# Kernel tuning notes

Hardware: AMD Instinct MI355X
Metric: run time of the kernel (lower is better)

Reference implementation:

```python
import jax, jax.numpy as jnp
import numpy as np

B, S, H, NH, HD = 2, 2048, 2048, 16, 128
E, TOPK, I = 8, 2, 2048
EPS = 1e-5
ROPE_THETA = 10000.0


def setup_inputs() -> dict:
    key = jax.random.key(0)
    ks = jax.random.split(key, 11)
    s = 0.02
    return {
        "hidden_states": jax.random.normal(ks[0], (B, S, H), jnp.float32),
        "position_ids": jnp.broadcast_to(jnp.arange(S, dtype=jnp.int32), (B, S)),
        "rms1_w": jnp.ones((H,), jnp.float32),
        "rms2_w": jnp.ones((H,), jnp.float32),
        "q_w": jax.random.normal(ks[1], (H, H), jnp.float32) * s,
        "k_w": jax.random.normal(ks[2], (H, H), jnp.float32) * s,
        "v_w": jax.random.normal(ks[3], (H, H), jnp.float32) * s,
        "o_w": jax.random.normal(ks[4], (H, H), jnp.float32) * s,
        "router_w": jax.random.normal(ks[5], (H, E), jnp.float32) * s,
        "w1": jax.random.normal(ks[6], (E, H, I), jnp.float32) * s,
        "w2": jax.random.normal(ks[7], (E, I, H), jnp.float32) * s,
        "w3": jax.random.normal(ks[8], (E, H, I), jnp.float32) * s,
    }


def rmsnorm(x, w):
    var = jnp.mean(x * x, axis=-1, keepdims=True)
    return (x * jax.lax.rsqrt(var + EPS)) * w


def rope(x, pos):
    # x: [B,S,NH,HD], pos: [B,S]
    half = HD // 2
    inv_freq = 1.0 / (ROPE_THETA ** (jnp.arange(0, half, dtype=jnp.float32) / half))
    ang = pos.astype(jnp.float32)[..., None] * inv_freq  # [B,S,half]
    cos = jnp.cos(ang)[:, :, None, :]
    sin = jnp.sin(ang)[:, :, None, :]
    x1, x2 = x[..., :half], x[..., half:]
    return jnp.concatenate([x1 * cos - x2 * sin, x2 * cos + x1 * sin], axis=-1)


def attention(x, pos, q_w, k_w, v_w, o_w):
    q = (x @ q_w).reshape(B, S, NH, HD)
    k = (x @ k_w).reshape(B, S, NH, HD)
    v = (x @ v_w).reshape(B, S, NH, HD)
    q = rope(q, pos)
    k = rope(k, pos)
    scores = jnp.einsum("bqhd,bkhd->bhqk", q, k) / np.sqrt(HD).astype(np.float32)
    causal = jnp.tril(jnp.ones((S, S), bool))
    scores = jnp.where(causal, scores, jnp.finfo(scores.dtype).min)
    probs = jax.nn.softmax(scores, axis=-1)
    ctx = jnp.einsum("bhqk,bkhd->bqhd", probs, v).reshape(B, S, H)
    return ctx @ o_w


def moe(x, router_w, w1, w2, w3):
    t = x.reshape(B * S, H)
    probs = jax.nn.softmax(t @ router_w, axis=-1)  # [T,E]
    top_v, top_i = jax.lax.top_k(probs, TOPK)
    top_v = top_v / jnp.sum(top_v, axis=-1, keepdims=True)
    T = B * S
    coeff = jnp.zeros((T, E), x.dtype).at[jnp.arange(T)[:, None], top_i].set(top_v)
    y = jnp.zeros((T, H), x.dtype)
    for e in range(E):  # fixed small expert loop
        h = jax.nn.silu(t @ w1[e]) * (t @ w3[e])
        y = y + coeff[:, e:e + 1] * (h @ w2[e])
    return y.reshape(B, S, H)


def reference(hidden_states, position_ids, rms1_w, rms2_w, q_w, k_w, v_w, o_w,
              router_w, w1, w2, w3):
    residual = hidden_states
    h = rmsnorm(hidden_states, rms1_w).astype(hidden_states.dtype)
    h = attention(h, position_ids, q_w, k_w, v_w, o_w)
    h = residual + h
    residual = h
    h = rmsnorm(h, rms2_w).astype(h.dtype)
    h = moe(h, router_w, w1, w2, w3)
    return residual + h
```

## Files before the change

### kernel.cpp

```cpp
#include <hip/hip_runtime.h>
#include <hip/hip_bf16.h>

constexpr int CB   = 2;
constexpr int CS   = 2048;
constexpr int CH   = 2048;
constexpr int CNH  = 16;
constexpr int CHD  = 128;
constexpr int CE   = 8;
constexpr int CI   = 2048;
constexpr int CT   = CB * CS;
constexpr int CQKV = 3 * CH;

typedef __attribute__((ext_vector_type(8))) short short8;
typedef __attribute__((ext_vector_type(4))) float float4v;
typedef __attribute__((ext_vector_type(4))) unsigned short ushort4v;
typedef unsigned int uint32;

__device__ __forceinline__ float bf2f(unsigned short u) {
    union { unsigned int i; float f; } x; x.i = ((unsigned int)u) << 16; return x.f;
}
__device__ __forceinline__ unsigned short f2bf(float f) {
    union { float f; unsigned int i; } x; x.f = f;
    unsigned int r = x.i + 0x7fffu + ((x.i >> 16) & 1u);
    return (unsigned short)(r >> 16);
}
__device__ __forceinline__ uint32 packpair(uint32 r0, uint32 r1) {
    return __builtin_amdgcn_perm(r1, r0, 0x07060302u);
}
__device__ __forceinline__ uint32 rnebits(float f) {
    uint32 u = __float_as_uint(f);
    return u + 0x7fffu + ((u >> 16) & 1u);
}
__device__ __forceinline__ void split2(float f0, float f1, uint32& h, uint32& l) {
    uint32 r0 = rnebits(f0), r1 = rnebits(f1);
    h = packpair(r0, r1);
    float d0 = f0 - __uint_as_float(r0 & 0xffff0000u);
    float d1 = f1 - __uint_as_float(r1 & 0xffff0000u);
    l = packpair(rnebits(d0), rnebits(d1));
}
__device__ __forceinline__ void rne16_store(const float* fv, unsigned short* dst) {
    uint32 h[8];
    #pragma unroll
    for (int p = 0; p < 8; p++) h[p] = packpair(rnebits(fv[2 * p]), rnebits(fv[2 * p + 1]));
    ((uint4*)dst)[0] = make_uint4(h[0], h[1], h[2], h[3]);
    ((uint4*)dst)[1] = make_uint4(h[4], h[5], h[6], h[7]);
}

template<int MODE>
__global__ __launch_bounds__(256) void rmsnorm_k(const float* __restrict__ x,
                                                 const float* __restrict__ w,
                                                 unsigned short* __restrict__ o1,
                                                 unsigned short* __restrict__ o2) {
    const int row = blockIdx.x;
    const float* xr = x + (size_t)row * CH;
    const int base = threadIdx.x * 8;
    float4 v0 = *(const float4*)(xr + base);
    float4 v1 = *(const float4*)(xr + base + 4);
    float ss = v0.x*v0.x + v0.y*v0.y + v0.z*v0.z + v0.w*v0.w
             + v1.x*v1.x + v1.y*v1.y + v1.z*v1.z + v1.w*v1.w;
    #pragma unroll
    for (int o = 1; o < 64; o <<= 1) ss += __shfl_xor(ss, o);
    __shared__ float ps[4];
    if ((threadIdx.x & 63) == 0) ps[threadIdx.x >> 6] = ss;
    __syncthreads();
    const float scale = rsqrtf((ps[0] + ps[1] + ps[2] + ps[3]) / (float)CH + 1e-5f);
    float4 w0 = *(const float4*)(w + base);
    float4 w1 = *(const float4*)(w + base + 4);
    float r[8] = {v0.x * scale * w0.x, v0.y * scale * w0.y, v0.z * scale * w0.z, v0.w * scale * w0.w,
                  v1.x * scale * w1.x, v1.y * scale * w1.y, v1.z * scale * w1.z, v1.w * scale * w1.w};
    if (MODE == 1) {
        rne16_store(r, o1 + (size_t)row * CH + base);
    } else {
        uint32 h[4], l[4];
        #pragma unroll
        for (int p = 0; p < 4; p++) split2(r[2 * p], r[2 * p + 1], h[p], l[p]);
        *(uint4*)(o1 + (size_t)row * CH + base) = make_uint4(h[0], h[1], h[2], h[3]);
        *(uint4*)(o2 + (size_t)row * CH + base) = make_uint4(l[0], l[1], l[2], l[3]);
    }
}

__global__ void rope_tab_k(float2* __restrict__ tab) {
    int i = blockIdx.x * 256 + threadIdx.x;
    int p = i >> 6, j = i & 63;
    double inv = pow(10000.0, -(double)j / 64.0);
    float invf = (float)inv;
    float angf = (float)p * invf;
    double da = (double)angf;
    tab[i] = make_float2((float)cos(da), (float)sin(da));
}

__global__ __launch_bounds__(256) void rope_k(unsigned short* __restrict__ qh,
                                              unsigned short* __restrict__ ql,
                                              const int* __restrict__ pos,
                                              const float2* __restrict__ tab) {
    int i = blockIdx.x * 256 + threadIdx.x;
    if (i >= CT * CNH * 64) return;
    int t = i >> 10, hj = i & 1023, hh = hj >> 6, j = hj & 63;
    float2 cs = tab[(size_t)pos[t] * 64 + j];
    unsigned short* qhp = qh + (size_t)t * CQKV + hh * CHD;
    unsigned short* qlp = ql + (size_t)t * CQKV + hh * CHD;
    #pragma unroll
    for (int s = 0; s < 2; s++) {
        unsigned short* hp = qhp + s * CH;
        unsigned short* lp = qlp + s * CH;
        float x1 = bf2f(hp[j]) + bf2f(lp[j]);
        float x2 = bf2f(hp[j + 64]) + bf2f(lp[j + 64]);
        float y1 = x1 * cs.x - x2 * cs.y;
        float y2 = x2 * cs.x + x1 * cs.y;
        uint32 r1 = rnebits(y1), r2 = rnebits(y2);
        hp[j]      = (unsigned short)(r1 >> 16);
        hp[j + 64] = (unsigned short)(r2 >> 16);
        lp[j]      = f2bf(y1 - __uint_as_float(r1 & 0xffff0000u));
        lp[j + 64] = f2bf(y2 - __uint_as_float(r2 & 0xffff0000u));
    }
}

template<int NMAT>
__global__ __launch_bounds__(256) void conv_k(const float* __restrict__ S0,
                                              const float* __restrict__ S1,
                                              unsigned short* __restrict__ D) {
    __shared__ float t[64][65];
    const int n0 = blockIdx.x * 64, k0 = blockIdx.y * 64, e = blockIdx.z;
    const size_t esrc = (size_t)e * 2048 * 2048;
    const int cc = threadIdx.x & 63, r4 = threadIdx.x >> 6;
    const int nl = threadIdx.x >> 2, q = threadIdx.x & 3;
    #pragma unroll
    for (int s = 0; s < NMAT; s++) {
        const float* S = s ? S1 : S0;
        __syncthreads();
        #pragma unroll
        for (int j = 0; j < 16; j++) {
            const int row = j * 4 + r4;
            t[cc][row] = S[esrc + (size_t)(k0 + row) * 2048 + n0 + cc];
        }
        __syncthreads();
        const int orow = (NMAT == 2) ? (2 * (n0 + nl) + s) : (n0 + nl);
        unsigned short* dp = D + (size_t)e * (NMAT * 2048) * 2048 + (size_t)orow * 2048 + k0 + q * 16;
        float fv[16];
        #pragma unroll
        for (int j = 0; j < 16; j++) fv[j] = t[nl][q * 16 + j];
        rne16_store(fv, dp);
    }
}

template<int NMAT>
__global__ __launch_bounds__(256) void convs_k(const float* __restrict__ S0,
                                               const float* __restrict__ S1,
                                               const float* __restrict__ S2,
                                               unsigned short* __restrict__ Dh,
                                               unsigned short* __restrict__ Dl) {
    __shared__ float t[64][65];
    const int n0 = blockIdx.x * 64, k0 = blockIdx.y * 64, z = blockIdx.z;
    const float* S = S0;
    if (NMAT == 3) S = (z == 0) ? S0 : ((z == 1) ? S1 : S2);
    const int cc = threadIdx.x & 63, r4 = threadIdx.x >> 6;
    #pragma unroll
    for (int j = 0; j < 16; j++) {
        const int row = j * 4 + r4;
        t[cc][row] = S[(size_t)(k0 + row) * 2048 + n0 + cc];
    }
    __syncthreads();
    const int nl = threadIdx.x >> 2, q = threadIdx.x & 3;
    float fv[16];
    #pragma unroll
    for (int j = 0; j < 16; j++) fv[j] = t[nl][q * 16 + j];
    uint32 h[8], l[8];
    #pragma unroll
    for (int p = 0; p < 8; p++) split2(fv[2 * p], fv[2 * p + 1], h[p], l[p]);
    const size_t off = (size_t)(z * 2048 + n0 + nl) * 2048 + k0 + q * 16;
    ((uint4*)(Dh + off))[0] = make_uint4(h[0], h[1], h[2], h[3]);
    ((uint4*)(Dh + off))[1] = make_uint4(h[4], h[5], h[6], h[7]);
    ((uint4*)(Dl + off))[0] = make_uint4(l[0], l[1], l[2], l[3]);
    ((uint4*)(Dl + off))[1] = make_uint4(l[4], l[5], l[6], l[7]);
}

template<int MODE>
__global__ __launch_bounds__(256) void sgemm_k(
    const unsigned short* __restrict__ Ahg, const unsigned short* __restrict__ Alg, int lda,
    const unsigned short* __restrict__ Bhg, const unsigned short* __restrict__ Blg, int K,
    unsigned short* __restrict__ Ch, unsigned short* __restrict__ Cl,
    float* __restrict__ Cf, int ldc,
    const float* __restrict__ resid, float* __restrict__ C2) {
    __shared__ unsigned short AhS[128][40], AlS[128][40], BhS[128][40], BlS[128][40];
    const int mt = blockIdx.x, nt = blockIdx.y, tid = threadIdx.x;
    const int m0 = mt * 128;
    const int srow = tid >> 1, shalf = tid & 1;
    const unsigned short* ah = Ahg + (size_t)(m0 + srow) * lda + shalf * 16;
    const unsigned short* al = Alg + (size_t)(m0 + srow) * lda + shalf * 16;
    const unsigned short* bhp = Bhg + (size_t)(nt * 128 + srow) * K + shalf * 16;
    const unsigned short* blp = Blg + (size_t)(nt * 128 + srow) * K + shalf * 16;
    const int lane = tid & 63, lr = lane & 15, lg = lane >> 4;
    const int wr = (tid >> 7) & 1, wc = (tid >> 6) & 1;

    float4v acc[4][4];
    #pragma unroll
    for (int m = 0; m < 4; m++)
        #pragma unroll
        for (int n = 0; n < 4; n++) acc[m][n] = (float4v){0.f, 0.f, 0.f, 0.f};

    short8 rah0 = *(const short8*)(ah),     rah1 = *(const short8*)(ah + 8);
    short8 ral0 = *(const short8*)(al),     ral1 = *(const short8*)(al + 8);
    short8 rbh0 = *(const short8*)(bhp),    rbh1 = *(const short8*)(bhp + 8);
    short8 rbl0 = *(const short8*)(blp),    rbl1 = *(const short8*)(blp + 8);

    for (int k0 = 0; k0 < K; k0 += 32) {
        __syncthreads();
        *(short8*)(&AhS[srow][shalf * 16])     = rah0;
        *(short8*)(&AhS[srow][shalf * 16 + 8]) = rah1;
        *(short8*)(&AlS[srow][shalf * 16])     = ral0;
        *(short8*)(&AlS[srow][shalf * 16 + 8]) = ral1;
        *(short8*)(&BhS[srow][shalf * 16])     = rbh0;
        *(short8*)(&BhS[srow][shalf * 16 + 8]) = rbh1;
        *(short8*)(&BlS[srow][shalf * 16])     = rbl0;
        *(short8*)(&BlS[srow][shalf * 16 + 8]) = rbl1;
        if (k0 + 32 < K) {
            rah0 = *(const short8*)(ah + k0 + 32);  rah1 = *(const short8*)(ah + k0 + 40);
            ral0 = *(const short8*)(al + k0 + 32);  ral1 = *(const short8*)(al + k0 + 40);
            rbh0 = *(const short8*)(bhp + k0 + 32); rbh1 = *(const short8*)(bhp + k0 + 40);
            rbl0 = *(const short8*)(blp + k0 + 32); rbl1 = *(const short8*)(blp + k0 + 40);
        }
        __syncthreads();
        short8 fah[4], fal[4], fbh[4], fbl[4];
        #pragma unroll
        for (int m = 0; m < 4; m++) {
            fah[m] = *(const short8*)(&AhS[wr * 64 + m * 16 + lr][lg * 8]);
            fal[m] = *(const short8*)(&AlS[wr * 64 + m * 16 + lr][lg * 8]);
        }
        #pragma unroll
        for (int n = 0; n < 4; n++) {
            fbh[n] = *(const short8*)(&BhS[wc * 64 + n * 16 + lr][lg * 8]);
            fbl[n] = *(const short8*)(&BlS[wc * 64 + n * 16 + lr][lg * 8]);
        }
        #pragma unroll
        for (int n = 0; n < 4; n++)
            #pragma unroll
            for (int m = 0; m < 4; m++) {
                acc[m][n] = __builtin_amdgcn_mfma_f32_16x16x32_bf16(fal[m], fbh[n], acc[m][n], 0, 0, 0);
                acc[m][n] = __builtin_amdgcn_mfma_f32_16x16x32_bf16(fah[m], fbl[n], acc[m][n], 0, 0, 0);
                acc[m][n] = __builtin_amdgcn_mfma_f32_16x16x32_bf16(fah[m], fbh[n], acc[m][n], 0, 0, 0);
            }
    }
    #pragma unroll
    for (int m = 0; m < 4; m++) {
        const int rb = wr * 64 + m * 16 + lg * 4;
        #pragma unroll
        for (int n = 0; n < 4; n++) {
            const int ccol = nt * 128 + wc * 64 + n * 16 + lr;
            #pragma unroll
            for (int r = 0; r < 4; r++) {
                const size_t idx = (size_t)(m0 + rb + r) * ldc + ccol;
                if (MODE == 1) {
                    const float v = acc[m][n][r] + resid[idx];
                    Cf[idx] = v;
                    C2[idx] = v;
                } else {
                    const float v = acc[m][n][r];
                    uint32 rr = rnebits(v);
                    Ch[idx] = (unsigned short)(rr >> 16);
                    Cl[idx] = f2bf(v - __uint_as_float(rr & 0xffff0000u));
                }
            }
        }
    }
}

template<int MODE>
__global__ __launch_bounds__(256) void gemm_k(
    const unsigned short* __restrict__ A, int lda,
    const unsigned short* __restrict__ Bt, int K, int Ne,
    void* __restrict__ Cp, int ldc,
    const int* __restrict__ cnt, const int* __restrict__ tokl,
    const float* __restrict__ gatel, const int* __restrict__ pb) {
    __shared__ unsigned short As[128][40];
    __shared__ unsigned short Bs[128][40];
    const int nt = blockIdx.x, mt = blockIdx.y, e = blockIdx.z;
    const int m0 = mt * 128;
    const int c = cnt[e];
    if (m0 >= c) return;
    const int valid = (c - m0 < 128) ? (c - m0) : 128;
    const int tid = threadIdx.x;
    const int srow = tid >> 1, shalf = tid & 1;
    size_t gr;
    if (MODE == 2) {
        const int idx = m0 + (srow < valid ? srow : valid - 1);
        gr = (size_t)tokl[e * 4096 + idx];
    } else {
        const int rr = m0 + srow;
        gr = (size_t)(pb[e] + (rr < c ? rr : c - 1));
    }
    const unsigned short* a_src = A + gr * (size_t)lda + shalf * 16;
    const unsigned short* b_src = Bt + (size_t)e * Ne * K + (size_t)(nt * 128 + srow) * K + shalf * 16;
    const int lane = tid & 63, lr = lane & 15, lg = lane >> 4;
    const int wr = (tid >> 7) & 1, wc = (tid >> 6) & 1;

    float4v acc[4][4];
    #pragma unroll
    for (int m = 0; m < 4; m++)
        #pragma unroll
        for (int n = 0; n < 4; n++) acc[m][n] = (float4v){0.f, 0.f, 0.f, 0.f};

    short8 ra0 = *(const short8*)(a_src);
    short8 ra1 = *(const short8*)(a_src + 8);
    short8 rb0 = *(const short8*)(b_src);
    short8 rb1 = *(const short8*)(b_src + 8);

    for (int k0 = 0; k0 < K; k0 += 32) {
        __syncthreads();
        *(short8*)(&As[srow][shalf * 16])     = ra0;
        *(short8*)(&As[srow][shalf * 16 + 8]) = ra1;
        *(short8*)(&Bs[srow][shalf * 16])     = rb0;
        *(short8*)(&Bs[srow][shalf * 16 + 8]) = rb1;
        if (k0 + 32 < K) {
            ra0 = *(const short8*)(a_src + k0 + 32);
            ra1 = *(const short8*)(a_src + k0 + 40);
            rb0 = *(const short8*)(b_src + k0 + 32);
            rb1 = *(const short8*)(b_src + k0 + 40);
        }
        __syncthreads();
        short8 af[4], bf[4];
        #pragma unroll
        for (int m = 0; m < 4; m++) af[m] = *(const short8*)(&As[wr * 64 + m * 16 + lr][lg * 8]);
        #pragma unroll
        for (int n = 0; n < 4; n++) bf[n] = *(const short8*)(&Bs[wc * 64 + n * 16 + lr][lg * 8]);
        #pragma unroll
        for (int n = 0; n < 4; n++)
            #pragma unroll
            for (int m = 0; m < 4; m++)
                acc[m][n] = __builtin_amdgcn_mfma_f32_16x16x32_bf16(af[m], bf[n], acc[m][n], 0, 0, 0);
    }

    #pragma unroll
    for (int m = 0; m < 4; m++) {
        const int rb = wr * 64 + m * 16 + lg * 4;
        #pragma unroll
        for (int n = 0; n < 4; n++) {
            const int col = nt * 128 + wc * 64 + n * 16 + lr;
            #pragma unroll
            for (int r = 0; r < 4; r++) {
                const int row = rb + r;
                const float v = acc[m][n][r];
                if (MODE == 2) {
                    const float other = __shfl_xor(v, 1);
                    if (!(lr & 1) && row < valid) {
                        const float g1 = v, g3 = other;
                        const float hsw = (g1 / (1.f + __expf(-g1))) * g3;
                        ((unsigned short*)Cp)[(size_t)(pb[e] + m0 + row) * ldc + (col >> 1)] = f2bf(hsw);
                    }
                } else {
                    if (row < valid) {
                        const int t = tokl[e * 4096 + m0 + row];
                        const float g = gatel[e * 4096 + m0 + row];
                        atomicAdd(((float*)Cp) + (size_t)t * ldc + col, v * g);
                    }
                }
            }
        }
    }
}

__global__ __launch_bounds__(256) void attn_k(const unsigned short* __restrict__ qh,
                                              const unsigned short* __restrict__ ql,
                                              unsigned short* __restrict__ ch,
                                              unsigned short* __restrict__ cl) {
    __shared__ unsigned short Ksh[32][136], Ksl[32][136];
    __shared__ unsigned short Vth[128][40], Vtl[128][40];
    const int bid = blockIdx.x;
    const int xcd = bid & 7, jj = bid >> 3;
    const int bh  = xcd * 4 + (jj >> 5);
    const int qb  = 31 - (jj & 31);
    const int h   = bh & 15, b = bh >> 4;
    const int tid = threadIdx.x;
    const int wave = tid >> 6, lane = tid & 63, lr = lane & 15, lg = lane >> 4;
    const size_t tb = (size_t)b * CS;
    const int q0 = qb * 64 + wave * 16;

    short8 qfh[4], qfl[4];
    {
        const size_t off = (tb + q0 + lr) * CQKV + h * CHD;
        #pragma unroll
        for (int c = 0; c < 4; c++) {
            qfh[c] = *(const short8*)(qh + off + c * 32 + lg * 8);
            qfl[c] = *(const short8*)(ql + off + c * 32 + lg * 8);
        }
    }
    float4v o[8];
    #pragma unroll
    for (int d = 0; d < 8; d++) o[d] = (float4v){0.f, 0.f, 0.f, 0.f};
    float m = -1e30f, l = 0.f;
    const float scl = 0.08838834764831845f;
    const int ntiles = 2 * (qb + 1);
    const int kk = tid >> 3, slot = tid & 7;
    const int vd = tid & 127, vhalf = tid >> 7;

    short8 pkh0, pkh1, pkl0, pkl1;
    unsigned short pth[16], ptl[16];
    {
        const size_t koff = (tb + kk) * CQKV + CH + h * CHD + slot * 16;
        pkh0 = *(const short8*)(qh + koff);
        pkh1 = *(const short8*)(qh + koff + 8);
        pkl0 = *(const short8*)(ql + koff);
        pkl1 = *(const short8*)(ql + koff + 8);
        const size_t voff = (tb + vhalf * 16) * CQKV + 2 * CH + h * CHD + vd;
        #pragma unroll
        for (int j = 0; j < 16; j++) {
            pth[j] = qh[voff + (size_t)j * CQKV];
            ptl[j] = ql[voff + (size_t)j * CQKV];
        }
    }

    for (int kt = 0; kt < ntiles; ++kt) {
        const int kv0 = kt * 32;
        __syncthreads();
        *(short8*)(&Ksh[kk][slot * 16])     = pkh0;
        *(short8*)(&Ksh[kk][slot * 16 + 8]) = pkh1;
        *(short8*)(&Ksl[kk][slot * 16])     = pkl0;
        *(short8*)(&Ksl[kk][slot * 16 + 8]) = pkl1;
        #pragma unroll
        for (int p = 0; p < 2; p++) {
            *(ushort4v*)(&Vth[vd][vhalf * 16 + p * 8])     = *(ushort4v*)(&pth[p * 8]);
            *(ushort4v*)(&Vth[vd][vhalf * 16 + p * 8 + 4]) = *(ushort4v*)(&pth[p * 8 + 4]);
            *(ushort4v*)(&Vtl[vd][vhalf * 16 + p * 8])     = *(ushort4v*)(&ptl[p * 8]);
            *(ushort4v*)(&Vtl[vd][vhalf * 16 + p * 8 + 4]) = *(ushort4v*)(&ptl[p * 8 + 4]);
        }
        if (kt + 1 < ntiles) {
            const int nv0 = kv0 + 32;
            const size_t koff = (tb + nv0 + kk) * CQKV + CH + h * CHD + slot * 16;
            pkh0 = *(const short8*)(qh + koff);
            pkh1 = *(const short8*)(qh + koff + 8);
            pkl0 = *(const short8*)(ql + koff);
            pkl1 = *(const short8*)(ql + koff + 8);
            const size_t voff = (tb + nv0 + vhalf * 16) * CQKV + 2 * CH + h * CHD + vd;
            #pragma unroll
            for (int j = 0; j < 16; j++) {
                pth[j] = qh[voff + (size_t)j * CQKV];
                ptl[j] = ql[voff + (size_t)j * CQKV];
            }
        }
        __syncthreads();

        float4v st0 = (float4v){0.f,0.f,0.f,0.f}, st1 = st0;
        #pragma unroll
        for (int c = 0; c < 4; c++) {
            short8 kah = *(const short8*)(&Ksh[lr][c * 32 + lg * 8]);
            short8 kal = *(const short8*)(&Ksl[lr][c * 32 + lg * 8]);
            short8 kbh = *(const short8*)(&Ksh[16 + lr][c * 32 + lg * 8]);
            short8 kbl = *(const short8*)(&Ksl[16 + lr][c * 32 + lg * 8]);
            st0 = __builtin_amdgcn_mfma_f32_16x16x32_bf16(kal, qfh[c], st0, 0, 0, 0);
            st0 = __builtin_amdgcn_mfma_f32_16x16x32_bf16(kah, qfl[c], st0, 0, 0, 0);
            st0 = __builtin_amdgcn_mfma_f32_16x16x32_bf16(kah, qfh[c], st0, 0, 0, 0);
            st1 = __builtin_amdgcn_mfma_f32_16x16x32_bf16(kbl, qfh[c], st1, 0, 0, 0);
            st1 = __builtin_amdgcn_mfma_f32_16x16x32_bf16(kbh, qfl[c], st1, 0, 0, 0);
            st1 = __builtin_amdgcn_mfma_f32_16x16x32_bf16(kbh, qfh[c], st1, 0, 0, 0);
        }
        float pv[8]; float pmax = -1e30f;
        const int qg = q0 + lr;
        #pragma unroll
        for (int f = 0; f < 2; f++) {
            #pragma unroll
            for (int r = 0; r < 4; r++) {
                const int kg = kv0 + f * 16 + lg * 4 + r;
                const float s = (kg <= qg) ? ((f ? st1[r] : st0[r]) * scl) : -1e30f;
                pv[f * 4 + r] = s;
                pmax = fmaxf(pmax, s);
            }
        }
        pmax = fmaxf(pmax, __shfl_xor(pmax, 16));
        pmax = fmaxf(pmax, __shfl_xor(pmax, 32));
        const float mnew = fmaxf(m, pmax);
        const float alpha = __expf(m - mnew);
        float sum = 0.f;
        #pragma unroll
        for (int i = 0; i < 8; i++) { const float p = __expf(pv[i] - mnew); pv[i] = p; sum += p; }
        sum += __shfl_xor(sum, 16);
        sum += __shfl_xor(sum, 32);
        l = l * alpha + sum;
        m = mnew;
        #pragma unroll
        for (int d = 0; d < 8; d++) o[d] *= alpha;
        short8 pfh, pfl;
        unsigned short* pfhp = (unsigned short*)&pfh;
        unsigned short* pflp = (unsigned short*)&pfl;
        #pragma unroll
        for (int j = 0; j < 8; j++) {
            const int srcl = (((lg & 1) * 2 + (j >> 2)) << 4) | lr;
            const float a0 = __shfl(pv[j & 3], srcl);
            const float a1 = __shfl(pv[4 + (j & 3)], srcl);
            const float sel = (lg >= 2) ? a1 : a0;
            uint32 r = rnebits(sel);
            pfhp[j] = (unsigned short)(r >> 16);
            float d = sel - __uint_as_float(r & 0xffff0000u);
            pflp[j] = (unsigned short)(rnebits(d) >> 16);
        }
        #pragma unroll
        for (int dt = 0; dt < 8; dt++) {
            short8 vh = *(const short8*)(&Vth[dt * 16 + lr][lg * 8]);
            short8 vl = *(const short8*)(&Vtl[dt * 16 + lr][lg * 8]);
            o[dt] = __builtin_amdgcn_mfma_f32_16x16x32_bf16(vl, pfh, o[dt], 0, 0, 0);
            o[dt] = __builtin_amdgcn_mfma_f32_16x16x32_bf16(vh, pfl, o[dt], 0, 0, 0);
            o[dt] = __builtin_amdgcn_mfma_f32_16x16x32_bf16(vh, pfh, o[dt], 0, 0, 0);
        }
    }
    const float inv = 1.f / l;
    const size_t coff = (tb + q0 + lr) * CH + h * CHD + lg * 4;
    #pragma unroll
    for (int dt = 0; dt < 8; dt++) {
        ushort4v wh, wl;
        #pragma unroll
        for (int r = 0; r < 4; r++) {
            const float v = o[dt][r] * inv;
            uint32 rr = rnebits(v);
            wh[r] = (unsigned short)(rr >> 16);
            wl[r] = f2bf(v - __uint_as_float(rr & 0xffff0000u));
        }
        *(ushort4v*)(ch + coff + dt * 16) = wh;
        *(ushort4v*)(cl + coff + dt * 16) = wl;
    }
}

__global__ __launch_bounds__(64) void router_k(const float* __restrict__ x,
                                               const float* __restrict__ wn,
                                               const float* __restrict__ rw,
                                               int* __restrict__ cnt, int* __restrict__ tok,
                                               float* __restrict__ gate) {
    const int t = blockIdx.x;
    const int lane = threadIdx.x;
    const float* xr = x + (size_t)t * CH;
    double ss = 0.0;
    double acc[8] = {0,0,0,0,0,0,0,0};
    for (int i = lane * 4; i < CH; i += 256) {
        float4 v = *(const float4*)(xr + i);
        float4 wv = *(const float4*)(wn + i);
        ss += (double)v.x*v.x + (double)v.y*v.y + (double)v.z*v.z + (double)v.w*v.w;
        float xs[4] = {v.x, v.y, v.z, v.w};
        float ws4[4] = {wv.x, wv.y, wv.z, wv.w};
        #pragma unroll
        for (int dd = 0; dd < 4; dd++) {
            const double xn = (double)xs[dd] * (double)ws4[dd];
            const float* rr = rw + (size_t)(i + dd) * CE;
            #pragma unroll
            for (int e2 = 0; e2 < 8; e2++) acc[e2] += xn * (double)rr[e2];
        }
    }
    #pragma unroll
    for (int o = 1; o < 64; o <<= 1) ss += __shfl_xor(ss, o);
    #pragma unroll
    for (int e2 = 0; e2 < 8; e2++) {
        #pragma unroll
        for (int o = 1; o < 64; o <<= 1) acc[e2] += __shfl_xor(acc[e2], o);
    }
    if (lane == 0) {
        const double scale = rsqrt(ss / (double)CH + 1e-5);
        int e0 = 0;
        #pragma unroll
        for (int e2 = 1; e2 < 8; e2++) if (acc[e2] > acc[e0]) e0 = e2;
        int e1 = (e0 == 0) ? 1 : 0;
        #pragma unroll
        for (int e2 = 0; e2 < 8; e2++) if (e2 != e0 && acc[e2] > acc[e1]) e1 = e2;
        const double dl = scale * (acc[e1] - acc[e0]);
        const double p1r = exp(dl);
        const float g0 = (float)(1.0 / (1.0 + p1r));
        const float g1 = (float)(p1r / (1.0 + p1r));
        int pos0 = atomicAdd(&cnt[e0], 1);
        tok[e0 * 4096 + pos0] = t; gate[e0 * 4096 + pos0] = g0;
        int pos1 = atomicAdd(&cnt[e1], 1);
        tok[e1 * 4096 + pos1] = t; gate[e1 * 4096 + pos1] = g1;
    }
}

__global__ void prefix_k(const int* __restrict__ cnt, int* __restrict__ pb) {
    if (threadIdx.x == 0 && blockIdx.x == 0) {
        int s = 0;
        for (int e = 0; e < CE; e++) { pb[e] = s; s += cnt[e]; }
    }
}

extern "C" void kernel_launch(void* const* d_in, const int* in_sizes, int n_in,
                              void* d_out, int out_size, void* d_ws, size_t ws_size,
                              hipStream_t stream) {
    (void)in_sizes; (void)n_in; (void)out_size; (void)ws_size;
    const float* hidden = (const float*)d_in[0];
    const int*   posids = (const int*)d_in[1];
    const float* rms1w  = (const float*)d_in[2];
    const float* rms2w  = (const float*)d_in[3];
    const float* qw     = (const float*)d_in[4];
    const float* kw     = (const float*)d_in[5];
    const float* vw     = (const float*)d_in[6];
    const float* ow     = (const float*)d_in[7];
    const float* rw     = (const float*)d_in[8];
    const float* w1     = (const float*)d_in[9];
    const float* w2     = (const float*)d_in[10];
    const float* w3     = (const float*)d_in[11];
    float* out = (float*)d_out;

    char* ws = (char*)d_ws;
    unsigned short* h1h = (unsigned short*)ws;
    unsigned short* h1l = (unsigned short*)(ws + 16777216);
    unsigned short* woh = (unsigned short*)ws;
    unsigned short* wol = (unsigned short*)(ws + 8388608);
    unsigned short* h2  = (unsigned short*)ws;
    int*   tok  = (int*)(ws + 16777216);
    float* gate = (float*)(ws + 16777216 + 131072);
    int*   cnt  = (int*)(ws + 16777216 + 262144);
    int*   pb   = cnt + 16;
    unsigned short* qkvh = (unsigned short*)(ws + 33554432);
    unsigned short* qkvl = (unsigned short*)(ws + 83886080);
    unsigned short* wt13 = (unsigned short*)(ws + 33554432);
    unsigned short* wt2  = (unsigned short*)(ws + 33554432);
    unsigned short* wqkvh = (unsigned short*)(ws + 134217728);
    unsigned short* wqkvl = (unsigned short*)(ws + 134217728 + 25165824);
    unsigned short* ctxh = (unsigned short*)(ws + 134217728);
    unsigned short* ctxl = (unsigned short*)(ws + 150994944);
    float*          res2 = (float*)(ws + 167772160);
    unsigned short* Hbuf = (unsigned short*)(ws + 167772160);
    float2*         rtab = (float2*)(ws + 201326592);

    rope_tab_k<<<512, 256, 0, stream>>>(rtab);
    rmsnorm_k<0><<<CT, 256, 0, stream>>>(hidden, rms1w, h1h, h1l);
    convs_k<3><<<dim3(32, 32, 3), 256, 0, stream>>>(qw, kw, vw, wqkvh, wqkvl);
    sgemm_k<0><<<dim3(32, 48), 256, 0, stream>>>(h1h, h1l, CH, wqkvh, wqkvl, CH,
                                                 qkvh, qkvl, nullptr, CQKV, nullptr, nullptr);
    rope_k<<<16384, 256, 0, stream>>>(qkvh, qkvl, posids, rtab);
    convs_k<1><<<dim3(32, 32, 1), 256, 0, stream>>>(ow, nullptr, nullptr, woh, wol);
    attn_k<<<1024, 256, 0, stream>>>(qkvh, qkvl, ctxh, ctxl);
    sgemm_k<1><<<dim3(32, 16), 256, 0, stream>>>(ctxh, ctxl, CH, woh, wol, CH,
                                                 nullptr, nullptr, res2, CH, hidden, out);
    rmsnorm_k<1><<<CT, 256, 0, stream>>>(res2, rms2w, h2, nullptr);
    hipMemsetAsync(cnt, 0, 8 * sizeof(int), stream);
    router_k<<<CT, 64, 0, stream>>>(res2, rms2w, rw, cnt, tok, gate);
    prefix_k<<<1, 64, 0, stream>>>(cnt, pb);
    conv_k<2><<<dim3(32, 32, CE), 256, 0, stream>>>(w1, w3, wt13);
    gemm_k<2><<<dim3(32, 32, CE), 256, 0, stream>>>(h2, CH, wt13, CH, 2 * CI, Hbuf, CI,
                                                    cnt, tok, gate, pb);
    conv_k<1><<<dim3(32, 32, CE), 256, 0, stream>>>(w2, nullptr, wt2);
    gemm_k<3><<<dim3(16, 32, CE), 256, 0, stream>>>(Hbuf, CI, wt2, CI, CH, out, CH,
                                                    cnt, tok, gate, pb);
}
```

Before: 1.440 ms.

## Fuse RMSNorm with router, vectorize RoPE, deepen GEMM prefetch, skip attention rescale

Measured after the change: 1.406 ms. 2.4% less time.

```diff
diff --git a/kernel.cpp b/kernel.cpp
--- a/kernel.cpp
+++ b/kernel.cpp
@@ -46,7 +46,6 @@
     ((uint4*)dst)[1] = make_uint4(h[4], h[5], h[6], h[7]);
 }
 
-template<int MODE>
 __global__ __launch_bounds__(256) void rmsnorm_k(const float* __restrict__ x,
                                                  const float* __restrict__ w,
                                                  unsigned short* __restrict__ o1,
@@ -68,14 +67,78 @@
     float4 w1 = *(const float4*)(w + base + 4);
     float r[8] = {v0.x * scale * w0.x, v0.y * scale * w0.y, v0.z * scale * w0.z, v0.w * scale * w0.w,
                   v1.x * scale * w1.x, v1.y * scale * w1.y, v1.z * scale * w1.z, v1.w * scale * w1.w};
-    if (MODE == 1) {
-        rne16_store(r, o1 + (size_t)row * CH + base);
-    } else {
-        uint32 h[4], l[4];
-        #pragma unroll
-        for (int p = 0; p < 4; p++) split2(r[2 * p], r[2 * p + 1], h[p], l[p]);
-        *(uint4*)(o1 + (size_t)row * CH + base) = make_uint4(h[0], h[1], h[2], h[3]);
-        *(uint4*)(o2 + (size_t)row * CH + base) = make_uint4(l[0], l[1], l[2], l[3]);
+    uint32 h[4], l[4];
+    #pragma unroll
+    for (int p = 0; p < 4; p++) split2(r[2 * p], r[2 * p + 1], h[p], l[p]);
+    *(uint4*)(o1 + (size_t)row * CH + base) = make_uint4(h[0], h[1], h[2], h[3]);
+    *(uint4*)(o2 + (size_t)row * CH + base) = make_uint4(l[0], l[1], l[2], l[3]);
+}
+
+__global__ __launch_bounds__(256) void rmsrouter_k(const float* __restrict__ x,
+                                                   const float* __restrict__ w,
+                                                   const float* __restrict__ rw,
+                                                   unsigned short* __restrict__ h2,
+                                                   int* __restrict__ cnt,
+                                                   int* __restrict__ tok,
+                                                   float* __restrict__ gate) {
+    const int row = blockIdx.x;
+    const float* xr = x + (size_t)row * CH;
+    const int base = threadIdx.x * 8;
+    float4 v0 = *(const float4*)(xr + base);
+    float4 v1 = *(const float4*)(xr + base + 4);
+    float ss = v0.x*v0.x + v0.y*v0.y + v0.z*v0.z + v0.w*v0.w
+             + v1.x*v1.x + v1.y*v1.y + v1.z*v1.z + v1.w*v1.w;
+    #pragma unroll
+    for (int o = 1; o < 64; o <<= 1) ss += __shfl_xor(ss, o);
+    __shared__ float ps[4];
+    __shared__ double dacc[4][8];
+    const int wave = threadIdx.x >> 6, lane = threadIdx.x & 63;
+    if (lane == 0) ps[wave] = ss;
+    __syncthreads();
+    const float scale = rsqrtf((ps[0] + ps[1] + ps[2] + ps[3]) / (float)CH + 1e-5f);
+    float4 w0 = *(const float4*)(w + base);
+    float4 w1 = *(const float4*)(w + base + 4);
+    float r[8] = {v0.x * scale * w0.x, v0.y * scale * w0.y, v0.z * scale * w0.z, v0.w * scale * w0.w,
+                  v1.x * scale * w1.x, v1.y * scale * w1.y, v1.z * scale * w1.z, v1.w * scale * w1.w};
+    rne16_store(r, h2 + (size_t)row * CH + base);
+    const float vv[8] = {v0.x, v0.y, v0.z, v0.w, v1.x, v1.y, v1.z, v1.w};
+    const float ww[8] = {w0.x, w0.y, w0.z, w0.w, w1.x, w1.y, w1.z, w1.w};
+    double acc[8] = {0, 0, 0, 0, 0, 0, 0, 0};
+    #pragma unroll
+    for (int jj = 0; jj < 8; jj++) {
+        const double xn = (double)vv[jj] * (double)ww[jj];
+        const float* rr = rw + (size_t)(base + jj) * CE;
+        #pragma unroll
+        for (int e = 0; e < 8; e++) acc[e] += xn * (double)rr[e];
+    }
+    #pragma unroll
+    for (int e = 0; e < 8; e++) {
+        #pragma unroll
+        for (int o = 1; o < 64; o <<= 1) acc[e] += __shfl_xor(acc[e], o);
+    }
+    if (lane == 0) {
+        #pragma unroll
+        for (int e = 0; e < 8; e++) dacc[wave][e] = acc[e];
+    }
+    __syncthreads();
+    if (threadIdx.x == 0) {
+        double a[8];
+        #pragma unroll
+        for (int e = 0; e < 8; e++) a[e] = dacc[0][e] + dacc[1][e] + dacc[2][e] + dacc[3][e];
+        int e0 = 0;
+        #pragma unroll
+        for (int e = 1; e < 8; e++) if (a[e] > a[e0]) e0 = e;
+        int e1 = (e0 == 0) ? 1 : 0;
+        #pragma unroll
+        for (int e = 0; e < 8; e++) if (e != e0 && a[e] > a[e1]) e1 = e;
+        const double dl = (double)scale * (a[e1] - a[e0]);
+        const double p1r = exp(dl);
+        const float g0 = (float)(1.0 / (1.0 + p1r));
+        const float g1 = (float)(p1r / (1.0 + p1r));
+        int pos0 = atomicAdd(&cnt[e0], 1);
+        tok[e0 * 4096 + pos0] = row; gate[e0 * 4096 + pos0] = g0;
+        int pos1 = atomicAdd(&cnt[e1], 1);
+        tok[e1 * 4096 + pos1] = row; gate[e1 * 4096 + pos1] = g1;
     }
 }
 
@@ -94,24 +157,47 @@
                                               const int* __restrict__ pos,
                                               const float2* __restrict__ tab) {
     int i = blockIdx.x * 256 + threadIdx.x;
-    if (i >= CT * CNH * 64) return;
-    int t = i >> 10, hj = i & 1023, hh = hj >> 6, j = hj & 63;
-    float2 cs = tab[(size_t)pos[t] * 64 + j];
-    unsigned short* qhp = qh + (size_t)t * CQKV + hh * CHD;
-    unsigned short* qlp = ql + (size_t)t * CQKV + hh * CHD;
+    if (i >= CT * CNH * 8) return;
+    int t = i >> 7, r = i & 127, hh = r >> 3, jo = (r & 7) << 3;
+    const float2* tp = tab + (size_t)pos[t] * 64 + jo;
+    float4 tc0 = ((const float4*)tp)[0];
+    float4 tc1 = ((const float4*)tp)[1];
+    float4 tc2 = ((const float4*)tp)[2];
+    float4 tc3 = ((const float4*)tp)[3];
+    float cx[8] = {tc0.x, tc0.z, tc1.x, tc1.z, tc2.x, tc2.z, tc3.x, tc3.z};
+    float cy[8] = {tc0.y, tc0.w, tc1.y, tc1.w, tc2.y, tc2.w, tc3.y, tc3.w};
+    const size_t off = (size_t)t * CQKV + hh * CHD + jo;
     #pragma unroll
     for (int s = 0; s < 2; s++) {
-        unsigned short* hp = qhp + s * CH;
-        unsigned short* lp = qlp + s * CH;
-        float x1 = bf2f(hp[j]) + bf2f(lp[j]);
-        float x2 = bf2f(hp[j + 64]) + bf2f(lp[j + 64]);
-        float y1 = x1 * cs.x - x2 * cs.y;
-        float y2 = x2 * cs.x + x1 * cs.y;
-        uint32 r1 = rnebits(y1), r2 = rnebits(y2);
-        hp[j]      = (unsigned short)(r1 >> 16);
-        hp[j + 64] = (unsigned short)(r2 >> 16);
-        lp[j]      = f2bf(y1 - __uint_as_float(r1 & 0xffff0000u));
-        lp[j + 64] = f2bf(y2 - __uint_as_float(r2 & 0xffff0000u));
+        unsigned short* hp = qh + off + s * CH;
+        unsigned short* lp = ql + off + s * CH;
+        short8 x1h = *(short8*)hp,        x1l = *(short8*)lp;
+        short8 x2h = *(short8*)(hp + 64), x2l = *(short8*)(lp + 64);
+        const unsigned short* p1h = (const unsigned short*)&x1h;
+        const unsigned short* p1l = (const unsigned short*)&x1l;
+        const unsigned short* p2h = (const unsigned short*)&x2h;
+        const unsigned short* p2l = (const unsigned short*)&x2l;
+        short8 y1h, y1l, y2h, y2l;
+        unsigned short* q1h = (unsigned short*)&y1h;
+        unsigned short* q1l = (unsigned short*)&y1l;
+        unsigned short* q2h = (unsigned short*)&y2h;
+        unsigned short* q2l = (unsigned short*)&y2l;
+        #pragma unroll
+        for (int jj = 0; jj < 8; jj++) {
+            const float x1 = bf2f(p1h[jj]) + bf2f(p1l[jj]);
+            const float x2 = bf2f(p2h[jj]) + bf2f(p2l[jj]);
+            const float yy1 = x1 * cx[jj] - x2 * cy[jj];
+            const float yy2 = x2 * cx[jj] + x1 * cy[jj];
+            const uint32 r1 = rnebits(yy1), r2 = rnebits(yy2);
+            q1h[jj] = (unsigned short)(r1 >> 16);
+            q2h[jj] = (unsigned short)(r2 >> 16);
+            q1l[jj] = f2bf(yy1 - __uint_as_float(r1 & 0xffff0000u));
+            q2l[jj] = f2bf(yy2 - __uint_as_float(r2 & 0xffff0000u));
+        }
+        *(short8*)hp        = y1h;
+        *(short8*)(hp + 64) = y2h;
+        *(short8*)lp        = y1l;
+        *(short8*)(lp + 64) = y2l;
     }
 }
 
@@ -198,26 +284,32 @@
         #pragma unroll
         for (int n = 0; n < 4; n++) acc[m][n] = (float4v){0.f, 0.f, 0.f, 0.f};
 
-    short8 rah0 = *(const short8*)(ah),     rah1 = *(const short8*)(ah + 8);
-    short8 ral0 = *(const short8*)(al),     ral1 = *(const short8*)(al + 8);
-    short8 rbh0 = *(const short8*)(bhp),    rbh1 = *(const short8*)(bhp + 8);
-    short8 rbl0 = *(const short8*)(blp),    rbl1 = *(const short8*)(blp + 8);
+    short8 cah0 = *(const short8*)(ah),      cah1 = *(const short8*)(ah + 8);
+    short8 cal0 = *(const short8*)(al),      cal1 = *(const short8*)(al + 8);
+    short8 cbh0 = *(const short8*)(bhp),     cbh1 = *(const short8*)(bhp + 8);
+    short8 cbl0 = *(const short8*)(blp),     cbl1 = *(const short8*)(blp + 8);
+    short8 nah0 = *(const short8*)(ah + 32), nah1 = *(const short8*)(ah + 40);
+    short8 nal0 = *(const short8*)(al + 32), nal1 = *(const short8*)(al + 40);
+    short8 nbh0 = *(const short8*)(bhp + 32), nbh1 = *(const short8*)(bhp + 40);
+    short8 nbl0 = *(const short8*)(blp + 32), nbl1 = *(const short8*)(blp + 40);
 
     for (int k0 = 0; k0 < K; k0 += 32) {
         __syncthreads();
-        *(short8*)(&AhS[srow][shalf * 16])     = rah0;
-        *(short8*)(&AhS[srow][shalf * 16 + 8]) = rah1;
-        *(short8*)(&AlS[srow][shalf * 16])     = ral0;
-        *(short8*)(&AlS[srow][shalf * 16 + 8]) = ral1;
-        *(short8*)(&BhS[srow][shalf * 16])     = rbh0;
-        *(short8*)(&BhS[srow][shalf * 16 + 8]) = rbh1;
-        *(short8*)(&BlS[srow][shalf * 16])     = rbl0;
-        *(short8*)(&BlS[srow][shalf * 16 + 8]) = rbl1;
-        if (k0 + 32 < K) {
-            rah0 = *(const short8*)(ah + k0 + 32);  rah1 = *(const short8*)(ah + k0 + 40);
-            ral0 = *(const short8*)(al + k0 + 32);  ral1 = *(const short8*)(al + k0 + 40);
-            rbh0 = *(const short8*)(bhp + k0 + 32); rbh1 = *(const short8*)(bhp + k0 + 40);
-            rbl0 = *(const short8*)(blp + k0 + 32); rbl1 = *(const short8*)(blp + k0 + 40);
+        *(short8*)(&AhS[srow][shalf * 16])     = cah0;
+        *(short8*)(&AhS[srow][shalf * 16 + 8]) = cah1;
+        *(short8*)(&AlS[srow][shalf * 16])     = cal0;
+        *(short8*)(&AlS[srow][shalf * 16 + 8]) = cal1;
+        *(short8*)(&BhS[srow][shalf * 16])     = cbh0;
+        *(short8*)(&BhS[srow][shalf * 16 + 8]) = cbh1;
+        *(short8*)(&BlS[srow][shalf * 16])     = cbl0;
+        *(short8*)(&BlS[srow][shalf * 16 + 8]) = cbl1;
+        cah0 = nah0; cah1 = nah1; cal0 = nal0; cal1 = nal1;
+        cbh0 = nbh0; cbh1 = nbh1; cbl0 = nbl0; cbl1 = nbl1;
+        if (k0 + 64 < K) {
+            nah0 = *(const short8*)(ah + k0 + 64);  nah1 = *(const short8*)(ah + k0 + 72);
+            nal0 = *(const short8*)(al + k0 + 64);  nal1 = *(const short8*)(al + k0 + 72);
+            nbh0 = *(const short8*)(bhp + k0 + 64); nbh1 = *(const short8*)(bhp + k0 + 72);
+            nbl0 = *(const short8*)(blp + k0 + 64); nbl1 = *(const short8*)(blp + k0 + 72);
         }
         __syncthreads();
         short8 fah[4], fal[4], fbh[4], fbl[4];
@@ -299,22 +391,23 @@
         #pragma unroll
         for (int n = 0; n < 4; n++) acc[m][n] = (float4v){0.f, 0.f, 0.f, 0.f};
 
-    short8 ra0 = *(const short8*)(a_src);
-    short8 ra1 = *(const short8*)(a_src + 8);
-    short8 rb0 = *(const short8*)(b_src);
-    short8 rb1 = *(const short8*)(b_src + 8);
+    short8 ca0 = *(const short8*)(a_src),      ca1 = *(const short8*)(a_src + 8);
+    short8 cb0 = *(const short8*)(b_src),      cb1 = *(const short8*)(b_src + 8);
+    short8 na0 = *(const short8*)(a_src + 32), na1 = *(const short8*)(a_src + 40);
+    short8 nb0 = *(const short8*)(b_src + 32), nb1 = *(const short8*)(b_src + 40);
 
     for (int k0 = 0; k0 < K; k0 += 32) {
         __syncthreads();
-        *(short8*)(&As[srow][shalf * 16])     = ra0;
-        *(short8*)(&As[srow][shalf * 16 + 8]) = ra1;
-        *(short8*)(&Bs[srow][shalf * 16])     = rb0;
-        *(short8*)(&Bs[srow][shalf * 16 + 8]) = rb1;
-        if (k0 + 32 < K) {
-            ra0 = *(const short8*)(a_src + k0 + 32);
-            ra1 = *(const short8*)(a_src + k0 + 40);
-            rb0 = *(const short8*)(b_src + k0 + 32);
-            rb1 = *(const short8*)(b_src + k0 + 40);
+        *(short8*)(&As[srow][shalf * 16])     = ca0;
+        *(short8*)(&As[srow][shalf * 16 + 8]) = ca1;
+        *(short8*)(&Bs[srow][shalf * 16])     = cb0;
+        *(short8*)(&Bs[srow][shalf * 16 + 8]) = cb1;
+        ca0 = na0; ca1 = na1; cb0 = nb0; cb1 = nb1;
+        if (k0 + 64 < K) {
+            na0 = *(const short8*)(a_src + k0 + 64);
+            na1 = *(const short8*)(a_src + k0 + 72);
+            nb0 = *(const short8*)(b_src + k0 + 64);
+            nb1 = *(const short8*)(b_src + k0 + 72);
         }
         __syncthreads();
         short8 af[4], bf[4];
@@ -466,17 +559,20 @@
         }
         pmax = fmaxf(pmax, __shfl_xor(pmax, 16));
         pmax = fmaxf(pmax, __shfl_xor(pmax, 32));
-        const float mnew = fmaxf(m, pmax);
-        const float alpha = __expf(m - mnew);
+        if (!__all(pmax <= m)) {
+            const float mnew = fmaxf(m, pmax);
+            const float alpha = __expf(m - mnew);
+            l *= alpha;
+            #pragma unroll
+            for (int d = 0; d < 8; d++) o[d] *= alpha;
+            m = mnew;
+        }
         float sum = 0.f;
         #pragma unroll
-        for (int i = 0; i < 8; i++) { const float p = __expf(pv[i] - mnew); pv[i] = p; sum += p; }
+        for (int i = 0; i < 8; i++) { const float p = __expf(pv[i] - m); pv[i] = p; sum += p; }
         sum += __shfl_xor(sum, 16);
         sum += __shfl_xor(sum, 32);
-        l = l * alpha + sum;
-        m = mnew;
-        #pragma unroll
-        for (int d = 0; d < 8; d++) o[d] *= alpha;
+        l += sum;
         short8 pfh, pfl;
         unsigned short* pfhp = (unsigned short*)&pfh;
         unsigned short* pflp = (unsigned short*)&pfl;
@@ -514,56 +610,6 @@
         }
         *(ushort4v*)(ch + coff + dt * 16) = wh;
         *(ushort4v*)(cl + coff + dt * 16) = wl;
-    }
-}
-
-__global__ __launch_bounds__(64) void router_k(const float* __restrict__ x,
-                                               const float* __restrict__ wn,
-                                               const float* __restrict__ rw,
-                                               int* __restrict__ cnt, int* __restrict__ tok,
-                                               float* __restrict__ gate) {
-    const int t = blockIdx.x;
-    const int lane = threadIdx.x;
-    const float* xr = x + (size_t)t * CH;
-    double ss = 0.0;
-    double acc[8] = {0,0,0,0,0,0,0,0};
-    for (int i = lane * 4; i < CH; i += 256) {
-        float4 v = *(const float4*)(xr + i);
-        float4 wv = *(const float4*)(wn + i);
-        ss += (double)v.x*v.x + (double)v.y*v.y + (double)v.z*v.z + (double)v.w*v.w;
-        float xs[4] = {v.x, v.y, v.z, v.w};
-        float ws4[4] = {wv.x, wv.y, wv.z, wv.w};
-        #pragma unroll
-        for (int dd = 0; dd < 4; dd++) {
-            const double xn = (double)xs[dd] * (double)ws4[dd];
-            const float* rr = rw + (size_t)(i + dd) * CE;
-            #pragma unroll
-            for (int e2 = 0; e2 < 8; e2++) acc[e2] += xn * (double)rr[e2];
-        }
-    }
-    #pragma unroll
-    for (int o = 1; o < 64; o <<= 1) ss += __shfl_xor(ss, o);
-    #pragma unroll
-    for (int e2 = 0; e2 < 8; e2++) {
-        #pragma unroll
-        for (int o = 1; o < 64; o <<= 1) acc[e2] += __shfl_xor(acc[e2], o);
-    }
-    if (lane == 0) {
-        const double scale = rsqrt(ss / (double)CH + 1e-5);
-        int e0 = 0;
-        #pragma unroll
-        for (int e2 = 1; e2 < 8; e2++) if (acc[e2] > acc[e0]) e0 = e2;
-        int e1 = (e0 == 0) ? 1 : 0;
-        #pragma unroll
-        for (int e2 = 0; e2 < 8; e2++) if (e2 != e0 && acc[e2] > acc[e1]) e1 = e2;
-        const double dl = scale * (acc[e1] - acc[e0]);
-        const double p1r = exp(dl);
-        const float g0 = (float)(1.0 / (1.0 + p1r));
-        const float g1 = (float)(p1r / (1.0 + p1r));
-        int pos0 = atomicAdd(&cnt[e0], 1);
-        tok[e0 * 4096 + pos0] = t; gate[e0 * 4096 + pos0] = g0;
-        int pos1 = atomicAdd(&cnt[e1], 1);
-        tok[e1 * 4096 + pos1] = t; gate[e1 * 4096 + pos1] = g1;
     }
 }
 
@@ -615,18 +661,17 @@
     float2*         rtab = (float2*)(ws + 201326592);
 
     rope_tab_k<<<512, 256, 0, stream>>>(rtab);
-    rmsnorm_k<0><<<CT, 256, 0, stream>>>(hidden, rms1w, h1h, h1l);
+    rmsnorm_k<<<CT, 256, 0, stream>>>(hidden, rms1w, h1h, h1l);
     convs_k<3><<<dim3(32, 32, 3), 256, 0, stream>>>(qw, kw, vw, wqkvh, wqkvl);
     sgemm_k<0><<<dim3(32, 48), 256, 0, stream>>>(h1h, h1l, CH, wqkvh, wqkvl, CH,
                                                  qkvh, qkvl, nullptr, CQKV, nullptr, nullptr);
-    rope_k<<<16384, 256, 0, stream>>>(qkvh, qkvl, posids, rtab);
+    rope_k<<<2048, 256, 0, stream>>>(qkvh, qkvl, posids, rtab);
     convs_k<1><<<dim3(32, 32, 1), 256, 0, stream>>>(ow, nullptr, nullptr, woh, wol);
     attn_k<<<1024, 256, 0, stream>>>(qkvh, qkvl, ctxh, ctxl);
     sgemm_k<1><<<dim3(32, 16), 256, 0, stream>>>(ctxh, ctxl, CH, woh, wol, CH,
                                                  nullptr, nullptr, res2, CH, hidden, out);
-    rmsnorm_k<1><<<CT, 256, 0, stream>>>(res2, rms2w, h2, nullptr);
     hipMemsetAsync(cnt, 0, 8 * sizeof(int), stream);
-    router_k<<<CT, 64, 0, stream>>>(res2, rms2w, rw, cnt, tok, gate);
+    rmsrouter_k<<<CT, 256, 0, stream>>>(res2, rms2w, rw, h2, cnt, tok, gate);
     prefix_k<<<1, 64, 0, stream>>>(cnt, pb);
     conv_k<2><<<dim3(32, 32, CE), 256, 0, stream>>>(w1, w3, wt13);
     gemm_k<2><<<dim3(32, 32, CE), 256, 0, stream>>>(h2, CH, wt13, CH, 2 * CI, Hbuf, CI,
```
